# Optimization experiments

Hardware: AMD Instinct MI355X
Metric: run time of the kernel (lower is better)

## Reference

```python
import jax, jax.numpy as jnp
import numpy as np

NUM_CODE = 1024
CODE_DIM = 256
COMMITMENT_COST = 0.25
EPS = 1e-12


def _l2norm(v, axis=-1):
    n = jnp.sqrt(jnp.sum(v * v, axis=axis, keepdims=True))
    return v / jnp.maximum(n, EPS)


def setup_inputs() -> dict:
    key = jax.random.key(0)
    k1, k2 = jax.random.split(key)
    x = jax.random.normal(k1, (64, 8, 128, CODE_DIM), dtype=jnp.float32)
    # codebook init: uniform(-1/num_code, 1/num_code) as in torch
    cw = (jax.random.uniform(k2, (NUM_CODE, CODE_DIM), dtype=jnp.float32) * 2.0 - 1.0) / NUM_CODE
    return {"x": x, "codebook_weight": cw}


def reference(x, codebook_weight):
    # x: [B, C, T, D]
    xn = _l2norm(x)                              # normalized encoder output
    cb = _l2norm(codebook_weight)                # [N, D] normalized codebook
    # cosine similarity and nearest-code lookup
    sim = jnp.einsum('bctd,nd->bctn', xn, cb)    # [B, C, T, N]
    code_indices = jnp.argmax(sim, axis=-1)      # [B, C, T] int
    # one-hot @ codebook == direct gather of normalized codebook rows
    quantized = cb[code_indices]                 # [B, C, T, D]
    # VQ losses (both inputs already normalized, matching torch detach semantics in fwd value)
    e_latent = jnp.mean((quantized - xn) ** 2)
    q_latent = jnp.mean((quantized - xn) ** 2)
    loss = q_latent + COMMITMENT_COST * e_latent
    # straight-through estimator (forward value == quantized)
    quantized_st = xn + jax.lax.stop_gradient(quantized - xn)
    # perplexity from code usage histogram (mean of one-hot over B,C,T)
    total = code_indices.size
    counts = jnp.zeros((NUM_CODE,), jnp.float32).at[code_indices.reshape(-1)].add(1.0)
    avg_probs = counts / total
    perplexity = jnp.exp(-jnp.sum(avg_probs * jnp.log(avg_probs + 1e-10)))
    return (loss, quantized_st, perplexity, codebook_weight, code_indices)
```

## Files before the change

### kernel.cpp

```cpp
#include <hip/hip_runtime.h>
#include <math.h>

#define D 256
#define NCODE 1024
#define V_TOTAL 65536
#define EPSF 1e-12f



__global__ __launch_bounds__(256) void normalize_cb(const float* __restrict__ w,
                                                    float* __restrict__ cb_n,
                                                    float* __restrict__ cb_t) {
    const int wave = threadIdx.x >> 6;
    const int lane = threadIdx.x & 63;
    const int row  = blockIdx.x * 4 + wave;
    float4 wv = *(const float4*)(w + (size_t)row * D + lane * 4);
    float s = wv.x * wv.x + wv.y * wv.y + wv.z * wv.z + wv.w * wv.w;
    #pragma unroll
    for (int off = 32; off; off >>= 1) s += __shfl_xor(s, off);
    const float scale = 1.0f / fmaxf(sqrtf(s), EPSF);
    float4 o;
    o.x = wv.x * scale; o.y = wv.y * scale; o.z = wv.z * scale; o.w = wv.w * scale;
    *(float4*)(cb_n + (size_t)row * D + lane * 4) = o;
    const int k = lane * 4;
    cb_t[(size_t)(k + 0) * NCODE + row] = o.x;
    cb_t[(size_t)(k + 1) * NCODE + row] = o.y;
    cb_t[(size_t)(k + 2) * NCODE + row] = o.z;
    cb_t[(size_t)(k + 3) * NCODE + row] = o.w;
}

__global__ __launch_bounds__(256) void vq_main(const float* __restrict__ x,
                                               const float* __restrict__ cb_t,
                                               int* __restrict__ idx_ws,
                                               unsigned int* __restrict__ counts,
                                               float* __restrict__ loss_acc,
                                               float* __restrict__ out_idx_f) {
    __shared__ float xl[64 * 260];
    __shared__ float nrm_s[64];
    const int tid = threadIdx.x;
    const int v0  = blockIdx.x * 64;

    const float4* xg = (const float4*)(x + (size_t)v0 * D);
    #pragma unroll
    for (int i = 0; i < 16; ++i) {
        const int f  = tid + i * 256;
        const int m  = f >> 6;
        const int kk = (f & 63) << 2;
        float4 val = xg[f];
        *(float4*)&xl[m * 260 + kk] = val;
    }
    __syncthreads();

    {
        const int row = tid >> 2, part = tid & 3;
        float ss = 0.f;
        #pragma unroll
        for (int q = 0; q < 16; ++q) {
            float4 xv = *(const float4*)&xl[row * 260 + part * 64 + q * 4];
            ss += xv.x * xv.x + xv.y * xv.y + xv.z * xv.z + xv.w * xv.w;
        }
        ss += __shfl_xor(ss, 1);
        ss += __shfl_xor(ss, 2);
        if (part == 0) nrm_s[row] = fmaxf(sqrtf(ss), EPSF);
    }
    __syncthreads();

    const int tn = tid & 15, tm = tid >> 4;
    float best[4]; int bidx[4];
    #pragma unroll
    for (int i = 0; i < 4; ++i) { best[i] = -3.4e38f; bidx[i] = 0; }

    const float* bp = cb_t + tn * 8;

    #pragma unroll 1
    for (int c = 0; c < 8; ++c) {
        const int n0 = c * 128 + tn * 8;
        const float* bc = bp + c * 128;
        float acc[4][8];
        #pragma unroll
        for (int i = 0; i < 4; ++i)
            #pragma unroll
            for (int j = 0; j < 8; ++j) acc[i][j] = 0.f;

        #pragma unroll 2
        for (int k4 = 0; k4 < 64; ++k4) {
            float4 xa[4];
            #pragma unroll
            for (int i = 0; i < 4; ++i)
                xa[i] = *(const float4*)&xl[(tm * 4 + i) * 260 + k4 * 4];
            #pragma unroll
            for (int kk = 0; kk < 4; ++kk) {
                const float* bk = bc + (size_t)(k4 * 4 + kk) * NCODE;
                float4 b0 = *(const float4*)bk;
                float4 b1 = *(const float4*)(bk + 4);
                #pragma unroll
                for (int i = 0; i < 4; ++i) {
                    const float xv = ((const float*)&xa[i])[kk];
                    acc[i][0] = fmaf(xv, b0.x, acc[i][0]);
                    acc[i][1] = fmaf(xv, b0.y, acc[i][1]);
                    acc[i][2] = fmaf(xv, b0.z, acc[i][2]);
                    acc[i][3] = fmaf(xv, b0.w, acc[i][3]);
                    acc[i][4] = fmaf(xv, b1.x, acc[i][4]);
                    acc[i][5] = fmaf(xv, b1.y, acc[i][5]);
                    acc[i][6] = fmaf(xv, b1.z, acc[i][6]);
                    acc[i][7] = fmaf(xv, b1.w, acc[i][7]);
                }
            }
        }
        #pragma unroll
        for (int i = 0; i < 4; ++i)
            #pragma unroll
            for (int j = 0; j < 8; ++j) {
                if (acc[i][j] > best[i]) { best[i] = acc[i][j]; bidx[i] = n0 + j; }
            }
    }

    #pragma unroll
    for (int off = 8; off; off >>= 1) {
        #pragma unroll
        for (int i = 0; i < 4; ++i) {
            float ov = __shfl_xor(best[i], off);
            int   oi = __shfl_xor(bidx[i], off);
            if (ov > best[i] || (ov == best[i] && oi < bidx[i])) { best[i] = ov; bidx[i] = oi; }
        }
    }

    float lpart = 0.f;
    if (tn == 0) {
        #pragma unroll
        for (int i = 0; i < 4; ++i) {
            const int row = tm * 4 + i;
            const int v   = v0 + row;
            const float sim = best[i] / nrm_s[row];
            lpart += 2.f - 2.f * sim;
            idx_ws[v] = bidx[i];
            out_idx_f[v] = (float)bidx[i];
            atomicAdd(&counts[bidx[i]], 1u);
        }
    }
    #pragma unroll
    for (int off = 32; off; off >>= 1) lpart += __shfl_xor(lpart, off);
    if ((tid & 63) == 0) atomicAdd(loss_acc, lpart);
}

__global__ __launch_bounds__(256) void gather_q(const int* __restrict__ idx_ws,
                                                const float* __restrict__ cb_n,
                                                float* __restrict__ outq) {
    const int wave = threadIdx.x >> 6;
    const int lane = threadIdx.x & 63;
    const int v = blockIdx.x * 4 + wave;
    const int idx = idx_ws[v];
    float4 val = *(const float4*)(cb_n + (size_t)idx * D + lane * 4);
    *(float4*)(outq + (size_t)v * D + lane * 4) = val;
}

__global__ __launch_bounds__(1024) void finalize(const unsigned int* __restrict__ counts,
                                                 const float* __restrict__ loss_acc,
                                                 float* __restrict__ out_loss,
                                                 float* __restrict__ out_perp) {
    __shared__ float red[16];
    const int t = threadIdx.x;
    const float p = (float)counts[t] / 65536.0f;
    float term = p * logf(p + 1e-10f);
    #pragma unroll
    for (int off = 32; off; off >>= 1) term += __shfl_xor(term, off);
    if ((t & 63) == 0) red[t >> 6] = term;
    __syncthreads();
    if (t < 16) {
        float s = red[t];
        #pragma unroll
        for (int off = 8; off; off >>= 1) s += __shfl_xor(s, off);
        if (t == 0) {
            *out_perp = expf(-s);
            *out_loss = 1.25f * (*loss_acc) / 16777216.0f;
        }
    }
}

extern "C" void kernel_launch(void* const* d_in, const int* in_sizes, int n_in,
                              void* d_out, int out_size, void* d_ws, size_t ws_size,
                              hipStream_t stream) {
    const float* x  = (const float*)d_in[0];
    const float* cw = (const float*)d_in[1];
    float* out = (float*)d_out;
    float* ws  = (float*)d_ws;

    float* cb_n          = ws;
    float* cb_t          = ws + 262144;
    int* idx_ws          = (int*)(ws + 524288);
    unsigned int* counts = (unsigned int*)(ws + 589824);
    float* loss_acc      = ws + 590848;

    hipMemsetAsync(counts, 0, (1024 + 1) * sizeof(float), stream);

    normalize_cb<<<256, 256, 0, stream>>>(cw, cb_n, cb_t);
    vq_main<<<1024, 256, 0, stream>>>(x, cb_t, idx_ws, counts, loss_acc,
                                      out + 17039362);
    gather_q<<<16384, 256, 0, stream>>>(idx_ws, cb_n, out + 1);
    finalize<<<1, 1024, 0, stream>>>(counts, loss_acc, out, out + 16777217);
    hipMemcpyAsync(out + 16777218, cw, (size_t)NCODE * D * sizeof(float),
                   hipMemcpyDeviceToDevice, stream);
}
```

Measured before the change: 604.6 us.

## Use split-bf16 MFMA GEMM with top-2 margin check and fp32 fallback

Replaces the fp32 FMA similarity GEMM with bf16 MFMA matrix instructions. Operands are split into hi/lo bf16 pairs (three products) to recover near-fp32 accuracy, and the packed x is staged in the output buffer as scratch. The GEMM keeps the top-2 similarities per row. A resolve kernel recomputes the exact fp32 argmax over all codes only when the top-2 gap is below a relative margin. The same kernel fuses the gather, counts, loss and index output, which adds extra pack passes over x and risks wrong picks when rounding error exceeds the margin.

```diff
diff --git a/kernel.cpp b/kernel.cpp
--- a/kernel.cpp
+++ b/kernel.cpp
@@ -3,14 +3,22 @@
 
 #define D 256
 #define NCODE 1024
-#define V_TOTAL 65536
+#define NROW 65536
 #define EPSF 1e-12f
-
-
+#define MARGIN_REL 4e-4f
+
+typedef __attribute__((ext_vector_type(8))) short short8;
+typedef __attribute__((ext_vector_type(4))) float f32x4;
+
+
+__device__ __forceinline__ unsigned short bf16rne(float v) {
+    unsigned u = __float_as_uint(v);
+    unsigned r = u + 0x7FFFu + ((u >> 16) & 1u);
+    return (unsigned short)(r >> 16);
+}
 
 __global__ __launch_bounds__(256) void normalize_cb(const float* __restrict__ w,
-                                                    float* __restrict__ cb_n,
-                                                    float* __restrict__ cb_t) {
+                                                    float* __restrict__ cb_n) {
     const int wave = threadIdx.x >> 6;
     const int lane = threadIdx.x & 63;
     const int row  = blockIdx.x * 4 + wave;
@@ -22,136 +30,197 @@
     float4 o;
     o.x = wv.x * scale; o.y = wv.y * scale; o.z = wv.z * scale; o.w = wv.w * scale;
     *(float4*)(cb_n + (size_t)row * D + lane * 4) = o;
-    const int k = lane * 4;
-    cb_t[(size_t)(k + 0) * NCODE + row] = o.x;
-    cb_t[(size_t)(k + 1) * NCODE + row] = o.y;
-    cb_t[(size_t)(k + 2) * NCODE + row] = o.z;
-    cb_t[(size_t)(k + 3) * NCODE + row] = o.w;
-}
-
-__global__ __launch_bounds__(256) void vq_main(const float* __restrict__ x,
-                                               const float* __restrict__ cb_t,
-                                               int* __restrict__ idx_ws,
+}
+
+__device__ __forceinline__ void pack_tile(const float* __restrict__ src, short8* __restrict__ dst,
+                                          int tile, int ks, int lane) {
+    const float* p = src + (size_t)(tile * 16 + (lane & 15)) * D + ks * 32 + ((lane >> 4) << 3);
+    float4 a = *(const float4*)p;
+    float4 b = *(const float4*)(p + 4);
+    float va[8] = {a.x, a.y, a.z, a.w, b.x, b.y, b.z, b.w};
+    short8 h, l;
+    #pragma unroll
+    for (int j = 0; j < 8; ++j) {
+        unsigned short hb = bf16rne(va[j]);
+        float hf = __uint_as_float((unsigned)hb << 16);
+        unsigned short lb = bf16rne(va[j] - hf);
+        h[j] = (short)hb; l[j] = (short)lb;
+    }
+    dst[(tile * 16 + ks) * 64 + lane]     = h;
+    dst[(tile * 16 + 8 + ks) * 64 + lane] = l;
+}
+
+__global__ __launch_bounds__(256) void pack_cb(const float* __restrict__ cb_n,
+                                               short8* __restrict__ cbp) {
+    const int wid = blockIdx.x * 4 + (threadIdx.x >> 6);
+    pack_tile(cb_n, cbp, wid >> 3, wid & 7, threadIdx.x & 63);
+}
+
+__global__ __launch_bounds__(256) void pack_x(const float* __restrict__ x,
+                                              short8* __restrict__ xp) {
+    const int wid = blockIdx.x * 4 + (threadIdx.x >> 6);
+    pack_tile(x, xp, wid >> 3, wid & 7, threadIdx.x & 63);
+}
+
+__global__ __launch_bounds__(256) void gemm_top2(const short8* __restrict__ xp,
+                                                 const short8* __restrict__ cbp,
+                                                 int* __restrict__ i1g,
+                                                 float* __restrict__ v1g,
+                                                 float* __restrict__ v2g) {
+    __shared__ float m1[2][64], m2[2][64];
+    __shared__ int   mi[2][64];
+    const int lane = threadIdx.x & 63, wave = threadIdx.x >> 6;
+    const int wm = wave >> 1, wn = wave & 1;
+    const int xtb = blockIdx.x * 8 + wn * 4;
+    const int g = lane >> 4;
+    const int cgrp = g * 4;
+
+    float rv1[4], rv2[4]; int ri1[4];
+    #pragma unroll
+    for (int i = 0; i < 4; ++i) { rv1[i] = -3.4e38f; rv2[i] = -3.4e38f; ri1[i] = 0; }
+
+    #pragma unroll 1
+    for (int p = 0; p < 8; ++p) {
+        f32x4 acc[4][4];
+        const f32x4 zero = {0.f, 0.f, 0.f, 0.f};
+        #pragma unroll
+        for (int i = 0; i < 4; ++i)
+            #pragma unroll
+            for (int j = 0; j < 4; ++j) acc[i][j] = zero;
+
+        const int ntb = p * 8 + wm * 4;
+
+        #pragma unroll 2
+        for (int t = 0; t < 24; ++t) {
+            const int cks = (t < 16) ? t : t - 16;
+            const int xks = (t < 8) ? t : t - 8;
+            short8 af[4], bx[4];
+            #pragma unroll
+            for (int fm = 0; fm < 4; ++fm)
+                af[fm] = cbp[((ntb + fm) * 16 + cks) * 64 + lane];
+            #pragma unroll
+            for (int fn = 0; fn < 4; ++fn)
+                bx[fn] = xp[((xtb + fn) * 16 + xks) * 64 + lane];
+            #pragma unroll
+            for (int fm = 0; fm < 4; ++fm)
+                #pragma unroll
+                for (int fn = 0; fn < 4; ++fn)
+                    acc[fm][fn] = __builtin_amdgcn_mfma_f32_16x16x32_bf16(
+                        af[fm], bx[fn], acc[fm][fn], 0, 0, 0);
+        }
+
+        const int cbase = p * 128 + wm * 64 + cgrp;
+        #pragma unroll
+        for (int fn = 0; fn < 4; ++fn) {
+            float lv1 = -3.4e38f, lv2 = -3.4e38f; int li1 = 0;
+            #pragma unroll
+            for (int fm = 0; fm < 4; ++fm)
+                #pragma unroll
+                for (int r = 0; r < 4; ++r) {
+                    const float v = acc[fm][fn][r];
+                    const int code = cbase + fm * 16 + r;
+                    if (v > lv1) { lv2 = lv1; lv1 = v; li1 = code; }
+                    else lv2 = fmaxf(lv2, v);
+                }
+            #pragma unroll
+            for (int off = 16; off <= 32; off <<= 1) {
+                const float ov1 = __shfl_xor(lv1, off);
+                const float ov2 = __shfl_xor(lv2, off);
+                const int   oi1 = __shfl_xor(li1, off);
+                if (ov1 > lv1 || (ov1 == lv1 && oi1 < li1)) {
+                    lv2 = fmaxf(lv1, ov2); lv1 = ov1; li1 = oi1;
+                } else {
+                    lv2 = fmaxf(lv2, ov1);
+                }
+            }
+            if (lv1 > rv1[fn]) { rv2[fn] = fmaxf(rv1[fn], lv2); rv1[fn] = lv1; ri1[fn] = li1; }
+            else               { rv2[fn] = fmaxf(rv2[fn], lv1); }
+        }
+    }
+
+    float w1 = (g == 0) ? rv1[0] : (g == 1) ? rv1[1] : (g == 2) ? rv1[2] : rv1[3];
+    float w2 = (g == 0) ? rv2[0] : (g == 1) ? rv2[1] : (g == 2) ? rv2[2] : rv2[3];
+    int   wi = (g == 0) ? ri1[0] : (g == 1) ? ri1[1] : (g == 2) ? ri1[2] : ri1[3];
+
+    if (wm == 1) { m1[wn][lane] = w1; m2[wn][lane] = w2; mi[wn][lane] = wi; }
+    __syncthreads();
+    if (wm == 0) {
+        const float o1 = m1[wn][lane], o2 = m2[wn][lane];
+        const int   oi = mi[wn][lane];
+        if (o1 > w1 || (o1 == w1 && oi < wi)) { w2 = fmaxf(w1, o2); w1 = o1; wi = oi; }
+        else                                  { w2 = fmaxf(w2, o1); }
+        const int row = blockIdx.x * 128 + wn * 64 + g * 16 + (lane & 15);
+        i1g[row] = wi; v1g[row] = w1; v2g[row] = w2;
+    }
+}
+
+__global__ __launch_bounds__(256) void resolve(const float* __restrict__ x,
+                                               const float* __restrict__ cb_n,
+                                               const int* __restrict__ i1g,
+                                               const float* __restrict__ v1g,
+                                               const float* __restrict__ v2g,
                                                unsigned int* __restrict__ counts,
                                                float* __restrict__ loss_acc,
-                                               float* __restrict__ out_idx_f) {
-    __shared__ float xl[64 * 260];
-    __shared__ float nrm_s[64];
-    const int tid = threadIdx.x;
-    const int v0  = blockIdx.x * 64;
-
-    const float4* xg = (const float4*)(x + (size_t)v0 * D);
-    #pragma unroll
-    for (int i = 0; i < 16; ++i) {
-        const int f  = tid + i * 256;
-        const int m  = f >> 6;
-        const int kk = (f & 63) << 2;
-        float4 val = xg[f];
-        *(float4*)&xl[m * 260 + kk] = val;
-    }
-    __syncthreads();
-
-    {
-        const int row = tid >> 2, part = tid & 3;
-        float ss = 0.f;
-        #pragma unroll
-        for (int q = 0; q < 16; ++q) {
-            float4 xv = *(const float4*)&xl[row * 260 + part * 64 + q * 4];
-            ss += xv.x * xv.x + xv.y * xv.y + xv.z * xv.z + xv.w * xv.w;
-        }
-        ss += __shfl_xor(ss, 1);
-        ss += __shfl_xor(ss, 2);
-        if (part == 0) nrm_s[row] = fmaxf(sqrtf(ss), EPSF);
-    }
-    __syncthreads();
-
-    const int tn = tid & 15, tm = tid >> 4;
-    float best[4]; int bidx[4];
-    #pragma unroll
-    for (int i = 0; i < 4; ++i) { best[i] = -3.4e38f; bidx[i] = 0; }
-
-    const float* bp = cb_t + tn * 8;
-
+                                               float* __restrict__ out_idx_f,
+                                               float* __restrict__ outq) {
+    __shared__ float xs[4][256];
+    const int lane = threadIdx.x & 63, wave = threadIdx.x >> 6;
+    float lloc = 0.f;
     #pragma unroll 1
-    for (int c = 0; c < 8; ++c) {
-        const int n0 = c * 128 + tn * 8;
-        const float* bc = bp + c * 128;
-        float acc[4][8];
-        #pragma unroll
-        for (int i = 0; i < 4; ++i)
-            #pragma unroll
-            for (int j = 0; j < 8; ++j) acc[i][j] = 0.f;
-
-        #pragma unroll 2
-        for (int k4 = 0; k4 < 64; ++k4) {
-            float4 xa[4];
-            #pragma unroll
-            for (int i = 0; i < 4; ++i)
-                xa[i] = *(const float4*)&xl[(tm * 4 + i) * 260 + k4 * 4];
-            #pragma unroll
-            for (int kk = 0; kk < 4; ++kk) {
-                const float* bk = bc + (size_t)(k4 * 4 + kk) * NCODE;
-                float4 b0 = *(const float4*)bk;
-                float4 b1 = *(const float4*)(bk + 4);
-                #pragma unroll
-                for (int i = 0; i < 4; ++i) {
-                    const float xv = ((const float*)&xa[i])[kk];
-                    acc[i][0] = fmaf(xv, b0.x, acc[i][0]);
-                    acc[i][1] = fmaf(xv, b0.y, acc[i][1]);
-                    acc[i][2] = fmaf(xv, b0.z, acc[i][2]);
-                    acc[i][3] = fmaf(xv, b0.w, acc[i][3]);
-                    acc[i][4] = fmaf(xv, b1.x, acc[i][4]);
-                    acc[i][5] = fmaf(xv, b1.y, acc[i][5]);
-                    acc[i][6] = fmaf(xv, b1.z, acc[i][6]);
-                    acc[i][7] = fmaf(xv, b1.w, acc[i][7]);
+    for (int row = blockIdx.x * 4 + wave; row < NROW; row += gridDim.x * 4) {
+        const float4 xv = *(const float4*)(x + (size_t)row * D + lane * 4);
+        float ss = xv.x * xv.x + xv.y * xv.y + xv.z * xv.z + xv.w * xv.w;
+        #pragma unroll
+        for (int off = 32; off; off >>= 1) ss += __shfl_xor(ss, off);
+        const float nrm = sqrtf(ss);
+
+        int idx = i1g[row];
+        const float gap = v1g[row] - v2g[row];
+        float dotv;
+        if (gap >= MARGIN_REL * nrm) {
+            const float4 cv = *(const float4*)(cb_n + (size_t)idx * D + lane * 4);
+            float d = xv.x * cv.x + xv.y * cv.y + xv.z * cv.z + xv.w * cv.w;
+            #pragma unroll
+            for (int off = 32; off; off >>= 1) d += __shfl_xor(d, off);
+            dotv = d;
+        } else {
+            *(float4*)&xs[wave][lane * 4] = xv;
+            asm volatile("s_waitcnt lgkmcnt(0)" ::: "memory");
+            float bv = -3.4e38f; int bi = 0;
+            #pragma unroll 1
+            for (int c = 0; c < 16; ++c) {
+                const int code = c * 64 + lane;
+                const float* cr = cb_n + (size_t)code * D;
+                float d = 0.f;
+                #pragma unroll 4
+                for (int k4 = 0; k4 < 64; ++k4) {
+                    const float4 cv = *(const float4*)(cr + k4 * 4);
+                    d = fmaf(xs[wave][k4 * 4 + 0], cv.x, d);
+                    d = fmaf(xs[wave][k4 * 4 + 1], cv.y, d);
+                    d = fmaf(xs[wave][k4 * 4 + 2], cv.z, d);
+                    d = fmaf(xs[wave][k4 * 4 + 3], cv.w, d);
                 }
+                if (d > bv) { bv = d; bi = code; }
             }
-        }
-        #pragma unroll
-        for (int i = 0; i < 4; ++i)
-            #pragma unroll
-            for (int j = 0; j < 8; ++j) {
-                if (acc[i][j] > best[i]) { best[i] = acc[i][j]; bidx[i] = n0 + j; }
+            #pragma unroll
+            for (int off = 32; off; off >>= 1) {
+                const float ov = __shfl_xor(bv, off);
+                const int   oi = __shfl_xor(bi, off);
+                if (ov > bv || (ov == bv && oi < bi)) { bv = ov; bi = oi; }
             }
-    }
-
-    #pragma unroll
-    for (int off = 8; off; off >>= 1) {
-        #pragma unroll
-        for (int i = 0; i < 4; ++i) {
-            float ov = __shfl_xor(best[i], off);
-            int   oi = __shfl_xor(bidx[i], off);
-            if (ov > best[i] || (ov == best[i] && oi < bidx[i])) { best[i] = ov; bidx[i] = oi; }
-        }
-    }
-
-    float lpart = 0.f;
-    if (tn == 0) {
-        #pragma unroll
-        for (int i = 0; i < 4; ++i) {
-            const int row = tm * 4 + i;
-            const int v   = v0 + row;
-            const float sim = best[i] / nrm_s[row];
-            lpart += 2.f - 2.f * sim;
-            idx_ws[v] = bidx[i];
-            out_idx_f[v] = (float)bidx[i];
-            atomicAdd(&counts[bidx[i]], 1u);
-        }
-    }
-    #pragma unroll
-    for (int off = 32; off; off >>= 1) lpart += __shfl_xor(lpart, off);
-    if ((tid & 63) == 0) atomicAdd(loss_acc, lpart);
-}
-
-__global__ __launch_bounds__(256) void gather_q(const int* __restrict__ idx_ws,
-                                                const float* __restrict__ cb_n,
-                                                float* __restrict__ outq) {
-    const int wave = threadIdx.x >> 6;
-    const int lane = threadIdx.x & 63;
-    const int v = blockIdx.x * 4 + wave;
-    const int idx = idx_ws[v];
-    float4 val = *(const float4*)(cb_n + (size_t)idx * D + lane * 4);
-    *(float4*)(outq + (size_t)v * D + lane * 4) = val;
+            idx = bi; dotv = bv;
+        }
+
+        const float sim = dotv / fmaxf(nrm, EPSF);
+        lloc += 2.f - 2.f * sim;
+        const float4 qv = *(const float4*)(cb_n + (size_t)idx * D + lane * 4);
+        *(float4*)(outq + (size_t)row * D + lane * 4) = qv;
+        if (lane == 0) {
+            atomicAdd(&counts[idx], 1u);
+            out_idx_f[row] = (float)idx;
+        }
+    }
+    if (lane == 0) atomicAdd(loss_acc, lloc);
 }
 
 __global__ __launch_bounds__(1024) void finalize(const unsigned int* __restrict__ counts,
@@ -185,18 +254,24 @@
     float* out = (float*)d_out;
     float* ws  = (float*)d_ws;
 
-    float* cb_n          = ws;
-    float* cb_t          = ws + 262144;
-    int* idx_ws          = (int*)(ws + 524288);
-    unsigned int* counts = (unsigned int*)(ws + 589824);
-    float* loss_acc      = ws + 590848;
-
-    hipMemsetAsync(counts, 0, (1024 + 1) * sizeof(float), stream);
-
-    normalize_cb<<<256, 256, 0, stream>>>(cw, cb_n, cb_t);
-    vq_main<<<1024, 256, 0, stream>>>(x, cb_t, idx_ws, counts, loss_acc,
-                                      out + 17039362);
-    gather_q<<<16384, 256, 0, stream>>>(idx_ws, cb_n, out + 1);
+    float*  cb_n         = ws;
+    short8* cbp          = (short8*)(ws + 262144);
+    int*    i1g          = (int*)(ws + 786432);
+    float*  v1g          = ws + 851968;
+    float*  v2g          = ws + 917504;
+    unsigned int* counts = (unsigned int*)(ws + 983040);
+    float*  loss_acc     = ws + 984064;
+
+    short8* xp = (short8*)(out + 4);
+
+    hipMemsetAsync(counts, 0, 1025 * sizeof(float), stream);
+
+    normalize_cb<<<256, 256, 0, stream>>>(cw, cb_n);
+    pack_cb<<<128, 256, 0, stream>>>(cb_n, cbp);
+    pack_x<<<8192, 256, 0, stream>>>(x, xp);
+    gemm_top2<<<512, 256, 0, stream>>>(xp, cbp, i1g, v1g, v2g);
+    resolve<<<2048, 256, 0, stream>>>(x, cb_n, i1g, v1g, v2g, counts, loss_acc,
+                                      out + 17039362, out + 1);
     finalize<<<1, 1024, 0, stream>>>(counts, loss_acc, out, out + 16777217);
     hipMemcpyAsync(out + 16777218, cw, (size_t)NCODE * D * sizeof(float),
                    hipMemcpyDeviceToDevice, stream);
```

Result: slower. 707.9 us (+17.1%).
